# Performance work log

Measured on AMD Instinct MI355X. Metric: run time of the kernel, lower is better.

Reference implementation:

```python
import jax, jax.numpy as jnp
import numpy as np

N, C, X, H = 50000, 8, 256, 256

def setup_inputs() -> dict:
    key = jax.random.key(0)
    k1, k2, k3, k4, k5, k6 = jax.random.split(key, 6)
    child_h = jax.random.normal(k1, (N, C, X), dtype=jnp.float32)
    parent_h = jax.random.normal(k2, (N, X), dtype=jnp.float32)
    u = lambda k, s: jax.random.uniform(k, s, jnp.float32, -0.1, 0.1)
    return {
        "child_h": child_h,
        "parent_h": parent_h,
        "W_left": u(k3, (X, H)),
        "W_right": u(k4, (X, H)),
        "W_top": u(k5, (X, H)),
        "b_conv": u(k6, (1, H)),
    }

def reference(child_h, parent_h, W_left, W_right, W_top, b_conv):
    # Positional continuous-binary-tree weights over C children:
    #   left_w[i]  = (C-1-i)/(C-1),  right_w[i] = i/(C-1)
    C_ = child_h.shape[1]
    i = jnp.arange(C_, dtype=child_h.dtype)
    left_w = (C_ - 1 - i) / (C_ - 1)   # [C]
    right_w = i / (C_ - 1)             # [C]
    # sum_i lw_i*(h_i @ W_l) + rw_i*(h_i @ W_r) == (sum_i lw_i h_i) @ W_l + (sum_i rw_i h_i) @ W_r
    s_left = jnp.einsum("ncx,c->nx", child_h, left_w)    # [N, X]
    s_right = jnp.einsum("ncx,c->nx", child_h, right_w)  # [N, X]
    children_state = s_left @ W_left + s_right @ W_right  # [N, H]
    return jax.nn.relu(children_state + parent_h @ W_top + b_conv)
```

## Files before the change

### kernel.cpp

```cpp
#include <hip/hip_runtime.h>
#include <hip/hip_bf16.h>

#define NROWS 50000
#define CDIM 8
#define XDIM 256
#define HDIM 256

typedef __attribute__((ext_vector_type(8))) short bf16x8;
typedef __attribute__((ext_vector_type(4))) float f32x4;

__device__ __forceinline__ unsigned short f2bf_rne(float f) {
    unsigned int u = __builtin_bit_cast(unsigned int, f);
    u += 0x7fffu + ((u >> 16) & 1u);
    return (unsigned short)(u >> 16);
}

__device__ __forceinline__ bf16x8 pack8(const f32x4 a, const f32x4 b) {
    bf16x8 r;
    r[0] = (short)f2bf_rne(a[0]);
    r[1] = (short)f2bf_rne(a[1]);
    r[2] = (short)f2bf_rne(a[2]);
    r[3] = (short)f2bf_rne(a[3]);
    r[4] = (short)f2bf_rne(b[0]);
    r[5] = (short)f2bf_rne(b[1]);
    r[6] = (short)f2bf_rne(b[2]);
    r[7] = (short)f2bf_rne(b[3]);
    return r;
}

__global__ __launch_bounds__(256) void pack_weights(
        const float* __restrict__ Wl, const float* __restrict__ Wr,
        const float* __restrict__ Wt, bf16x8* __restrict__ wp) {
    int t = blockIdx.x * 256 + threadIdx.x;
    int lane = t & 63;
    int tile = t >> 6;
    int ht  = tile & 15;
    int sx  = tile >> 4;
    int xc  = sx & 7;
    int seg = sx >> 3;
    const float* __restrict__ W = (seg == 0) ? Wl : (seg == 1) ? Wr : Wt;
    int x0 = xc * 32 + (lane >> 4) * 8;
    int h  = ht * 16 + (lane & 15);
    bf16x8 frag;
#pragma unroll
    for (int j = 0; j < 8; ++j)
        frag[j] = (short)f2bf_rne(W[(size_t)(x0 + j) * HDIM + h]);
    wp[t] = frag;
}

__global__ __launch_bounds__(256) void tbcnn_main(
        const float* __restrict__ child, const float* __restrict__ parent,
        const bf16x8* __restrict__ wp, const float* __restrict__ bias,
        float* __restrict__ out) {
    const int wave = threadIdx.x >> 6;
    const int lane = threadIdx.x & 63;
    const int wtask = blockIdx.x * 4 + wave;
    const int row0 = wtask * 16;
    if (row0 >= NROWS) return;

    const int rmod = lane & 15;
    const int quad = lane >> 4;
    const int row  = row0 + rmod;

    const float* __restrict__ chrow = child  + (size_t)row * (CDIM * XDIM);
    const float* __restrict__ prow  = parent + (size_t)row * XDIM;

    const float lwt[8] = {7.f/7.f, 6.f/7.f, 5.f/7.f, 4.f/7.f, 3.f/7.f, 2.f/7.f, 1.f/7.f, 0.f/7.f};
    const float rwt[8] = {0.f/7.f, 1.f/7.f, 2.f/7.f, 3.f/7.f, 4.f/7.f, 5.f/7.f, 6.f/7.f, 7.f/7.f};

    f32x4 acc[16];
#pragma unroll
    for (int t = 0; t < 16; ++t) acc[t] = (f32x4){0.f, 0.f, 0.f, 0.f};

#pragma unroll 1
    for (int xc = 0; xc < 8; ++xc) {
        const int x0 = xc * 32 + quad * 8;

        f32x4 sl0 = (f32x4){0.f,0.f,0.f,0.f}, sl1 = (f32x4){0.f,0.f,0.f,0.f};
        f32x4 sr0 = (f32x4){0.f,0.f,0.f,0.f}, sr1 = (f32x4){0.f,0.f,0.f,0.f};
#pragma unroll
        for (int c = 0; c < CDIM; ++c) {
            const f32x4* p = (const f32x4*)(chrow + (size_t)c * XDIM + x0);
            f32x4 a = p[0];
            f32x4 b = p[1];
            sl0 += a * lwt[c];  sl1 += b * lwt[c];
            sr0 += a * rwt[c];  sr1 += b * rwt[c];
        }
        const f32x4* pp = (const f32x4*)(prow + x0);
        f32x4 p0 = pp[0];
        f32x4 p1 = pp[1];

        bf16x8 fL = pack8(sl0, sl1);
        bf16x8 fR = pack8(sr0, sr1);
        bf16x8 fP = pack8(p0, p1);

        const bf16x8* wL = wp + ((size_t)((0 * 8 + xc) * 16)) * 64 + lane;
        const bf16x8* wR = wp + ((size_t)((1 * 8 + xc) * 16)) * 64 + lane;
        const bf16x8* wT = wp + ((size_t)((2 * 8 + xc) * 16)) * 64 + lane;
#pragma unroll
        for (int ht = 0; ht < 16; ++ht)
            acc[ht] = __builtin_amdgcn_mfma_f32_16x16x32_bf16(wL[ht * 64], fL, acc[ht], 0, 0, 0);
#pragma unroll
        for (int ht = 0; ht < 16; ++ht)
            acc[ht] = __builtin_amdgcn_mfma_f32_16x16x32_bf16(wR[ht * 64], fR, acc[ht], 0, 0, 0);
#pragma unroll
        for (int ht = 0; ht < 16; ++ht)
            acc[ht] = __builtin_amdgcn_mfma_f32_16x16x32_bf16(wT[ht * 64], fP, acc[ht], 0, 0, 0);
    }

    float* __restrict__ orow = out + (size_t)row * HDIM;
#pragma unroll
    for (int ht = 0; ht < 16; ++ht) {
        const int h = ht * 16 + quad * 4;
        f32x4 b4 = *(const f32x4*)(bias + h);
        f32x4 v = acc[ht];
        v[0] = fmaxf(v[0] + b4[0], 0.f);
        v[1] = fmaxf(v[1] + b4[1], 0.f);
        v[2] = fmaxf(v[2] + b4[2], 0.f);
        v[3] = fmaxf(v[3] + b4[3], 0.f);
        *(f32x4*)(orow + h) = v;
    }
}

__global__ __launch_bounds__(256) void tbcnn_fallback(
        const float* __restrict__ child, const float* __restrict__ parent,
        const float* __restrict__ Wl, const float* __restrict__ Wr,
        const float* __restrict__ Wt, const float* __restrict__ bias,
        float* __restrict__ out) {
    __shared__ float sl[XDIM], sr[XDIM], sp[XDIM];
    const int n = blockIdx.x;
    const int h = threadIdx.x;
    const float lwt[8] = {7.f/7.f, 6.f/7.f, 5.f/7.f, 4.f/7.f, 3.f/7.f, 2.f/7.f, 1.f/7.f, 0.f/7.f};
    const float* ch = child + (size_t)n * (CDIM * XDIM);
    float al = 0.f, ar = 0.f;
#pragma unroll
    for (int c = 0; c < CDIM; ++c) {
        float v = ch[c * XDIM + h];
        al += lwt[c] * v;
        ar += (1.f - lwt[c]) * v;
    }
    ar = 0.f;
    const float rwt[8] = {0.f/7.f, 1.f/7.f, 2.f/7.f, 3.f/7.f, 4.f/7.f, 5.f/7.f, 6.f/7.f, 7.f/7.f};
#pragma unroll
    for (int c = 0; c < CDIM; ++c) ar += rwt[c] * ch[c * XDIM + h];
    sl[h] = al; sr[h] = ar; sp[h] = parent[(size_t)n * XDIM + h];
    __syncthreads();
    float a = bias[h];
    for (int x = 0; x < XDIM; ++x)
        a += sl[x] * Wl[(size_t)x * HDIM + h] + sr[x] * Wr[(size_t)x * HDIM + h]
           + sp[x] * Wt[(size_t)x * HDIM + h];
    out[(size_t)n * HDIM + h] = fmaxf(a, 0.f);
}

extern "C" void kernel_launch(void* const* d_in, const int* in_sizes, int n_in,
                              void* d_out, int out_size, void* d_ws, size_t ws_size,
                              hipStream_t stream) {
    const float* child  = (const float*)d_in[0];
    const float* parent = (const float*)d_in[1];
    const float* Wl     = (const float*)d_in[2];
    const float* Wr     = (const float*)d_in[3];
    const float* Wt     = (const float*)d_in[4];
    const float* bias   = (const float*)d_in[5];
    float* out = (float*)d_out;

    const size_t wp_bytes = (size_t)3 * XDIM * HDIM * sizeof(unsigned short);
    if (ws_size >= wp_bytes) {
        bf16x8* wp = (bf16x8*)d_ws;
        pack_weights<<<96, 256, 0, stream>>>(Wl, Wr, Wt, wp);
        const int n_wtasks = NROWS / 16;
        const int n_blocks = (n_wtasks + 3) / 4;
        tbcnn_main<<<n_blocks, 256, 0, stream>>>(child, parent, wp, bias, out);
    } else {
        tbcnn_fallback<<<NROWS, 256, 0, stream>>>(child, parent, Wl, Wr, Wt, bias, out);
    }
}
```

Measured before the change: 658.8 us.

## Fuse weight packing into main kernel with per-block LDS staging of bf16 weights

Removes the separate pack_weights launch and the workspace buffer. Each block now converts its current x-chunk of the three fp32 weight matrices to bf16 MFMA fragments itself, stores them in shared memory, and the four waves read the B operands from LDS instead of global memory. This saves a kernel launch and the global re-reads of packed weights. In exchange, every block (782 of them) re-reads and re-converts the full fp32 weights with strided loads, and adds two __syncthreads per chunk.

```diff
diff --git a/kernel.cpp b/kernel.cpp
--- a/kernel.cpp
+++ b/kernel.cpp
@@ -1,5 +1,4 @@
 #include <hip/hip_runtime.h>
-#include <hip/hip_bf16.h>
 
 #define NROWS 50000
 #define CDIM 8
@@ -28,39 +27,22 @@
     return r;
 }
 
-__global__ __launch_bounds__(256) void pack_weights(
+__global__ __launch_bounds__(256) void tbcnn_fused(
+        const float* __restrict__ child, const float* __restrict__ parent,
         const float* __restrict__ Wl, const float* __restrict__ Wr,
-        const float* __restrict__ Wt, bf16x8* __restrict__ wp) {
-    int t = blockIdx.x * 256 + threadIdx.x;
-    int lane = t & 63;
-    int tile = t >> 6;
-    int ht  = tile & 15;
-    int sx  = tile >> 4;
-    int xc  = sx & 7;
-    int seg = sx >> 3;
-    const float* __restrict__ W = (seg == 0) ? Wl : (seg == 1) ? Wr : Wt;
-    int x0 = xc * 32 + (lane >> 4) * 8;
-    int h  = ht * 16 + (lane & 15);
-    bf16x8 frag;
-#pragma unroll
-    for (int j = 0; j < 8; ++j)
-        frag[j] = (short)f2bf_rne(W[(size_t)(x0 + j) * HDIM + h]);
-    wp[t] = frag;
-}
+        const float* __restrict__ Wt, const float* __restrict__ bias,
+        float* __restrict__ out) {
+    __shared__ bf16x8 wlds[3 * 16 * 64];
 
-__global__ __launch_bounds__(256) void tbcnn_main(
-        const float* __restrict__ child, const float* __restrict__ parent,
-        const bf16x8* __restrict__ wp, const float* __restrict__ bias,
-        float* __restrict__ out) {
-    const int wave = threadIdx.x >> 6;
-    const int lane = threadIdx.x & 63;
-    const int wtask = blockIdx.x * 4 + wave;
-    const int row0 = wtask * 16;
-    if (row0 >= NROWS) return;
+    const int tid  = threadIdx.x;
+    const int wave = tid >> 6;
+    const int lane = tid & 63;
+    const int row0 = (blockIdx.x * 4 + wave) * 16;
+    const bool active = (row0 < NROWS);
 
     const int rmod = lane & 15;
     const int quad = lane >> 4;
-    const int row  = row0 + rmod;
+    const int row  = active ? (row0 + rmod) : 0;
 
     const float* __restrict__ chrow = child  + (size_t)row * (CDIM * XDIM);
     const float* __restrict__ prow  = parent + (size_t)row * XDIM;
@@ -72,84 +54,79 @@
 #pragma unroll
     for (int t = 0; t < 16; ++t) acc[t] = (f32x4){0.f, 0.f, 0.f, 0.f};
 
+    const int fx = (lane >> 4) * 8;
+    const int fh = lane & 15;
+
 #pragma unroll 1
     for (int xc = 0; xc < 8; ++xc) {
         const int x0 = xc * 32 + quad * 8;
 
-        f32x4 sl0 = (f32x4){0.f,0.f,0.f,0.f}, sl1 = (f32x4){0.f,0.f,0.f,0.f};
-        f32x4 sr0 = (f32x4){0.f,0.f,0.f,0.f}, sr1 = (f32x4){0.f,0.f,0.f,0.f};
+        bf16x8 fL, fR, fP;
+        if (active) {
+            f32x4 sl0 = (f32x4){0.f,0.f,0.f,0.f}, sl1 = (f32x4){0.f,0.f,0.f,0.f};
+            f32x4 sr0 = (f32x4){0.f,0.f,0.f,0.f}, sr1 = (f32x4){0.f,0.f,0.f,0.f};
 #pragma unroll
-        for (int c = 0; c < CDIM; ++c) {
-            const f32x4* p = (const f32x4*)(chrow + (size_t)c * XDIM + x0);
-            f32x4 a = p[0];
-            f32x4 b = p[1];
-            sl0 += a * lwt[c];  sl1 += b * lwt[c];
-            sr0 += a * rwt[c];  sr1 += b * rwt[c];
+            for (int c = 0; c < CDIM; ++c) {
+                const f32x4* p = (const f32x4*)(chrow + (size_t)c * XDIM + x0);
+                f32x4 a = p[0];
+                f32x4 b = p[1];
+                sl0 += a * lwt[c];  sl1 += b * lwt[c];
+                sr0 += a * rwt[c];  sr1 += b * rwt[c];
+            }
+            const f32x4* pp = (const f32x4*)(prow + x0);
+            f32x4 p0 = pp[0];
+            f32x4 p1 = pp[1];
+            fL = pack8(sl0, sl1);
+            fR = pack8(sr0, sr1);
+            fP = pack8(p0, p1);
         }
-        const f32x4* pp = (const f32x4*)(prow + x0);
-        f32x4 p0 = pp[0];
-        f32x4 p1 = pp[1];
 
-        bf16x8 fL = pack8(sl0, sl1);
-        bf16x8 fR = pack8(sr0, sr1);
-        bf16x8 fP = pack8(p0, p1);
+#pragma unroll 2
+        for (int k = 0; k < 12; ++k) {
+            const int tile = k * 4 + wave;
+            const int ht  = tile & 15;
+            const int seg = tile >> 4;
+            const float* __restrict__ W = (seg == 0) ? Wl : (seg == 1) ? Wr : Wt;
+            const float* __restrict__ wp = W + (size_t)(xc * 32 + fx) * HDIM + (ht * 16 + fh);
+            bf16x8 fr;
+#pragma unroll
+            for (int j = 0; j < 8; ++j)
+                fr[j] = (short)f2bf_rne(wp[(size_t)j * HDIM]);
+            wlds[tile * 64 + lane] = fr;
+        }
+        __syncthreads();
 
-        const bf16x8* wL = wp + ((size_t)((0 * 8 + xc) * 16)) * 64 + lane;
-        const bf16x8* wR = wp + ((size_t)((1 * 8 + xc) * 16)) * 64 + lane;
-        const bf16x8* wT = wp + ((size_t)((2 * 8 + xc) * 16)) * 64 + lane;
+        if (active) {
+            const bf16x8* wLp = &wlds[(0 * 16) * 64 + lane];
+            const bf16x8* wRp = &wlds[(1 * 16) * 64 + lane];
+            const bf16x8* wTp = &wlds[(2 * 16) * 64 + lane];
 #pragma unroll
-        for (int ht = 0; ht < 16; ++ht)
-            acc[ht] = __builtin_amdgcn_mfma_f32_16x16x32_bf16(wL[ht * 64], fL, acc[ht], 0, 0, 0);
+            for (int ht = 0; ht < 16; ++ht)
+                acc[ht] = __builtin_amdgcn_mfma_f32_16x16x32_bf16(wLp[ht * 64], fL, acc[ht], 0, 0, 0);
 #pragma unroll
-        for (int ht = 0; ht < 16; ++ht)
-            acc[ht] = __builtin_amdgcn_mfma_f32_16x16x32_bf16(wR[ht * 64], fR, acc[ht], 0, 0, 0);
+            for (int ht = 0; ht < 16; ++ht)
+                acc[ht] = __builtin_amdgcn_mfma_f32_16x16x32_bf16(wRp[ht * 64], fR, acc[ht], 0, 0, 0);
 #pragma unroll
-        for (int ht = 0; ht < 16; ++ht)
-            acc[ht] = __builtin_amdgcn_mfma_f32_16x16x32_bf16(wT[ht * 64], fP, acc[ht], 0, 0, 0);
+            for (int ht = 0; ht < 16; ++ht)
+                acc[ht] = __builtin_amdgcn_mfma_f32_16x16x32_bf16(wTp[ht * 64], fP, acc[ht], 0, 0, 0);
+        }
+        __syncthreads();
     }
 
-    float* __restrict__ orow = out + (size_t)row * HDIM;
+    if (active) {
+        float* __restrict__ orow = out + (size_t)row * HDIM;
 #pragma unroll
-    for (int ht = 0; ht < 16; ++ht) {
-        const int h = ht * 16 + quad * 4;
-        f32x4 b4 = *(const f32x4*)(bias + h);
-        f32x4 v = acc[ht];
-        v[0] = fmaxf(v[0] + b4[0], 0.f);
-        v[1] = fmaxf(v[1] + b4[1], 0.f);
-        v[2] = fmaxf(v[2] + b4[2], 0.f);
-        v[3] = fmaxf(v[3] + b4[3], 0.f);
-        *(f32x4*)(orow + h) = v;
+        for (int ht = 0; ht < 16; ++ht) {
+            const int h = ht * 16 + quad * 4;
+            f32x4 b4 = *(const f32x4*)(bias + h);
+            f32x4 v = acc[ht];
+            v[0] = fmaxf(v[0] + b4[0], 0.f);
+            v[1] = fmaxf(v[1] + b4[1], 0.f);
+            v[2] = fmaxf(v[2] + b4[2], 0.f);
+            v[3] = fmaxf(v[3] + b4[3], 0.f);
+            *(f32x4*)(orow + h) = v;
+        }
     }
-}
-
-__global__ __launch_bounds__(256) void tbcnn_fallback(
-        const float* __restrict__ child, const float* __restrict__ parent,
-        const float* __restrict__ Wl, const float* __restrict__ Wr,
-        const float* __restrict__ Wt, const float* __restrict__ bias,
-        float* __restrict__ out) {
-    __shared__ float sl[XDIM], sr[XDIM], sp[XDIM];
-    const int n = blockIdx.x;
-    const int h = threadIdx.x;
-    const float lwt[8] = {7.f/7.f, 6.f/7.f, 5.f/7.f, 4.f/7.f, 3.f/7.f, 2.f/7.f, 1.f/7.f, 0.f/7.f};
-    const float* ch = child + (size_t)n * (CDIM * XDIM);
-    float al = 0.f, ar = 0.f;
-#pragma unroll
-    for (int c = 0; c < CDIM; ++c) {
-        float v = ch[c * XDIM + h];
-        al += lwt[c] * v;
-        ar += (1.f - lwt[c]) * v;
-    }
-    ar = 0.f;
-    const float rwt[8] = {0.f/7.f, 1.f/7.f, 2.f/7.f, 3.f/7.f, 4.f/7.f, 5.f/7.f, 6.f/7.f, 7.f/7.f};
-#pragma unroll
-    for (int c = 0; c < CDIM; ++c) ar += rwt[c] * ch[c * XDIM + h];
-    sl[h] = al; sr[h] = ar; sp[h] = parent[(size_t)n * XDIM + h];
-    __syncthreads();
-    float a = bias[h];
-    for (int x = 0; x < XDIM; ++x)
-        a += sl[x] * Wl[(size_t)x * HDIM + h] + sr[x] * Wr[(size_t)x * HDIM + h]
-           + sp[x] * Wt[(size_t)x * HDIM + h];
-    out[(size_t)n * HDIM + h] = fmaxf(a, 0.f);
 }
 
 extern "C" void kernel_launch(void* const* d_in, const int* in_sizes, int n_in,
@@ -163,14 +140,8 @@
     const float* bias   = (const float*)d_in[5];
     float* out = (float*)d_out;
 
-    const size_t wp_bytes = (size_t)3 * XDIM * HDIM * sizeof(unsigned short);
-    if (ws_size >= wp_bytes) {
-        bf16x8* wp = (bf16x8*)d_ws;
-        pack_weights<<<96, 256, 0, stream>>>(Wl, Wr, Wt, wp);
-        const int n_wtasks = NROWS / 16;
-        const int n_blocks = (n_wtasks + 3) / 4;
-        tbcnn_main<<<n_blocks, 256, 0, stream>>>(child, parent, wp, bias, out);
-    } else {
-        tbcnn_fallback<<<NROWS, 256, 0, stream>>>(child, parent, Wl, Wr, Wt, bias, out);
-    }
+    const int n_wtasks = NROWS / 16;
+    const int n_blocks = (n_wtasks + 3) / 4;
+    tbcnn_fused<<<n_blocks, 256, 0, stream>>>(child, parent, Wl, Wr, Wt, bias, out);
+    (void)d_ws; (void)ws_size;
 }
```

Measured after the change: 661.4 us. No clear change (+0.4%).

## Share activation fragments via LDS and split H across waves to cut weight traffic

Applied to the files above, without the earlier changes.

Each block of four waves now covers 64 rows. Each wave computes all 64 rows for a 64-column slice of H instead of 16 rows across all 256 columns. The packed bf16 activation fragments are exchanged through a double-buffered LDS array with one barrier per x-chunk, so each wave streams only a quarter of the packed weights per block. The next weight fragments are software-prefetched one segment ahead. The aim is to cut the repeated cache and memory traffic on weights, in exchange for LDS traffic, a block-wide barrier, and redundant work in the last partial block. The fallback kernel's right-weight sum is also tidied.

```diff
diff --git a/kernel.cpp b/kernel.cpp
--- a/kernel.cpp
+++ b/kernel.cpp
@@ -52,37 +52,49 @@
         const float* __restrict__ child, const float* __restrict__ parent,
         const bf16x8* __restrict__ wp, const float* __restrict__ bias,
         float* __restrict__ out) {
+    __shared__ bf16x8 flds[2][4][3][64];
+
     const int wave = threadIdx.x >> 6;
     const int lane = threadIdx.x & 63;
-    const int wtask = blockIdx.x * 4 + wave;
-    const int row0 = wtask * 16;
-    if (row0 >= NROWS) return;
-
     const int rmod = lane & 15;
     const int quad = lane >> 4;
-    const int row  = row0 + rmod;
 
-    const float* __restrict__ chrow = child  + (size_t)row * (CDIM * XDIM);
-    const float* __restrict__ prow  = parent + (size_t)row * XDIM;
+    const int blk0   = blockIdx.x * 64;
+    const int rb_own = blk0 + wave * 16;
+    const int row_own = ((rb_own + 16 <= NROWS) ? rb_own : (NROWS - 16)) + rmod;
+
+    const float* __restrict__ chrow = child  + (size_t)row_own * (CDIM * XDIM);
+    const float* __restrict__ prow  = parent + (size_t)row_own * XDIM;
 
     const float lwt[8] = {7.f/7.f, 6.f/7.f, 5.f/7.f, 4.f/7.f, 3.f/7.f, 2.f/7.f, 1.f/7.f, 0.f/7.f};
     const float rwt[8] = {0.f/7.f, 1.f/7.f, 2.f/7.f, 3.f/7.f, 4.f/7.f, 5.f/7.f, 6.f/7.f, 7.f/7.f};
 
-    f32x4 acc[16];
+    f32x4 acc[4][4];
 #pragma unroll
-    for (int t = 0; t < 16; ++t) acc[t] = (f32x4){0.f, 0.f, 0.f, 0.f};
+    for (int rt = 0; rt < 4; ++rt)
+#pragma unroll
+        for (int t = 0; t < 4; ++t) acc[rt][t] = (f32x4){0.f, 0.f, 0.f, 0.f};
+
+    bf16x8 wn[4];
+    {
+        const bf16x8* wb0 = wp + (size_t)((0 * 16 + wave * 4) * 64 + lane);
+#pragma unroll
+        for (int t = 0; t < 4; ++t) wn[t] = wb0[t * 64];
+    }
 
 #pragma unroll 1
     for (int xc = 0; xc < 8; ++xc) {
+        const int p  = xc & 1;
         const int x0 = xc * 32 + quad * 8;
+        const bf16x8* wb = wp + (size_t)((xc * 16 + wave * 4) * 64 + lane);
 
         f32x4 sl0 = (f32x4){0.f,0.f,0.f,0.f}, sl1 = (f32x4){0.f,0.f,0.f,0.f};
         f32x4 sr0 = (f32x4){0.f,0.f,0.f,0.f}, sr1 = (f32x4){0.f,0.f,0.f,0.f};
 #pragma unroll
         for (int c = 0; c < CDIM; ++c) {
-            const f32x4* p = (const f32x4*)(chrow + (size_t)c * XDIM + x0);
-            f32x4 a = p[0];
-            f32x4 b = p[1];
+            const f32x4* cp = (const f32x4*)(chrow + (size_t)c * XDIM + x0);
+            f32x4 a = cp[0];
+            f32x4 b = cp[1];
             sl0 += a * lwt[c];  sl1 += b * lwt[c];
             sr0 += a * rwt[c];  sr1 += b * rwt[c];
         }
@@ -90,35 +102,46 @@
         f32x4 p0 = pp[0];
         f32x4 p1 = pp[1];
 
-        bf16x8 fL = pack8(sl0, sl1);
-        bf16x8 fR = pack8(sr0, sr1);
-        bf16x8 fP = pack8(p0, p1);
+        flds[p][wave][0][lane] = pack8(sl0, sl1);
+        flds[p][wave][1][lane] = pack8(sr0, sr1);
+        flds[p][wave][2][lane] = pack8(p0, p1);
+        __syncthreads();
 
-        const bf16x8* wL = wp + ((size_t)((0 * 8 + xc) * 16)) * 64 + lane;
-        const bf16x8* wR = wp + ((size_t)((1 * 8 + xc) * 16)) * 64 + lane;
-        const bf16x8* wT = wp + ((size_t)((2 * 8 + xc) * 16)) * 64 + lane;
 #pragma unroll
-        for (int ht = 0; ht < 16; ++ht)
-            acc[ht] = __builtin_amdgcn_mfma_f32_16x16x32_bf16(wL[ht * 64], fL, acc[ht], 0, 0, 0);
+        for (int seg = 0; seg < 3; ++seg) {
+            bf16x8 wc[4];
 #pragma unroll
-        for (int ht = 0; ht < 16; ++ht)
-            acc[ht] = __builtin_amdgcn_mfma_f32_16x16x32_bf16(wR[ht * 64], fR, acc[ht], 0, 0, 0);
+            for (int t = 0; t < 4; ++t) wc[t] = wn[t];
+            const int noff = (seg < 2) ? (seg + 1) * 8192 : 1024;
 #pragma unroll
-        for (int ht = 0; ht < 16; ++ht)
-            acc[ht] = __builtin_amdgcn_mfma_f32_16x16x32_bf16(wT[ht * 64], fP, acc[ht], 0, 0, 0);
+            for (int t = 0; t < 4; ++t) wn[t] = wb[noff + t * 64];
+#pragma unroll
+            for (int rt = 0; rt < 4; ++rt) {
+                bf16x8 f = flds[p][rt][seg][lane];
+#pragma unroll
+                for (int t = 0; t < 4; ++t)
+                    acc[rt][t] = __builtin_amdgcn_mfma_f32_16x16x32_bf16(wc[t], f, acc[rt][t], 0, 0, 0);
+            }
+        }
     }
 
-    float* __restrict__ orow = out + (size_t)row * HDIM;
 #pragma unroll
-    for (int ht = 0; ht < 16; ++ht) {
-        const int h = ht * 16 + quad * 4;
-        f32x4 b4 = *(const f32x4*)(bias + h);
-        f32x4 v = acc[ht];
-        v[0] = fmaxf(v[0] + b4[0], 0.f);
-        v[1] = fmaxf(v[1] + b4[1], 0.f);
-        v[2] = fmaxf(v[2] + b4[2], 0.f);
-        v[3] = fmaxf(v[3] + b4[3], 0.f);
-        *(f32x4*)(orow + h) = v;
+    for (int rt = 0; rt < 4; ++rt) {
+        const int rb = blk0 + rt * 16;
+        if (rb + 16 <= NROWS) {
+            float* __restrict__ orow = out + (size_t)(rb + rmod) * HDIM;
+#pragma unroll
+            for (int t = 0; t < 4; ++t) {
+                const int h = (wave * 4 + t) * 16 + quad * 4;
+                f32x4 b4 = *(const f32x4*)(bias + h);
+                f32x4 v = acc[rt][t];
+                v[0] = fmaxf(v[0] + b4[0], 0.f);
+                v[1] = fmaxf(v[1] + b4[1], 0.f);
+                v[2] = fmaxf(v[2] + b4[2], 0.f);
+                v[3] = fmaxf(v[3] + b4[3], 0.f);
+                *(f32x4*)(orow + h) = v;
+            }
+        }
     }
 }
 
@@ -131,18 +154,15 @@
     const int n = blockIdx.x;
     const int h = threadIdx.x;
     const float lwt[8] = {7.f/7.f, 6.f/7.f, 5.f/7.f, 4.f/7.f, 3.f/7.f, 2.f/7.f, 1.f/7.f, 0.f/7.f};
+    const float rwt[8] = {0.f/7.f, 1.f/7.f, 2.f/7.f, 3.f/7.f, 4.f/7.f, 5.f/7.f, 6.f/7.f, 7.f/7.f};
     const float* ch = child + (size_t)n * (CDIM * XDIM);
     float al = 0.f, ar = 0.f;
 #pragma unroll
     for (int c = 0; c < CDIM; ++c) {
         float v = ch[c * XDIM + h];
         al += lwt[c] * v;
-        ar += (1.f - lwt[c]) * v;
+        ar += rwt[c] * v;
     }
-    ar = 0.f;
-    const float rwt[8] = {0.f/7.f, 1.f/7.f, 2.f/7.f, 3.f/7.f, 4.f/7.f, 5.f/7.f, 6.f/7.f, 7.f/7.f};
-#pragma unroll
-    for (int c = 0; c < CDIM; ++c) ar += rwt[c] * ch[c * XDIM + h];
     sl[h] = al; sr[h] = ar; sp[h] = parent[(size_t)n * XDIM + h];
     __syncthreads();
     float a = bias[h];
@@ -167,8 +187,7 @@
     if (ws_size >= wp_bytes) {
         bf16x8* wp = (bf16x8*)d_ws;
         pack_weights<<<96, 256, 0, stream>>>(Wl, Wr, Wt, wp);
-        const int n_wtasks = NROWS / 16;
-        const int n_blocks = (n_wtasks + 3) / 4;
+        const int n_blocks = (NROWS + 63) / 64;
         tbcnn_main<<<n_blocks, 256, 0, stream>>>(child, parent, wp, bias, out);
     } else {
         tbcnn_fallback<<<NROWS, 256, 0, stream>>>(child, parent, Wl, Wr, Wt, bias, out);
```

Result: faster. 612.4 us (-7.0%).
